# Optimization experiments

Measured on AMD Instinct MI355X. Metric: run time of the kernel, lower is better.

## Reference

```python
import jax, jax.numpy as jnp
import numpy as np

MASK_BIAS = 2.0
TEMPERATURE = 1.0


def setup_inputs() -> dict:
    key = jax.random.key(0)
    k1, k2, k3 = jax.random.split(key, 3)
    B, C, D, H, W = 2, 128, 48, 96, 96
    feat = jax.random.normal(k1, (B, C, D, H, W), dtype=jnp.float32)
    mask = jax.random.uniform(k2, (B, 1, D, H, W), dtype=jnp.float32)
    w_attn = jax.random.normal(k3, (C,), dtype=jnp.float32) * (1.0 / np.sqrt(C))
    return {"feat": feat, "mask": mask, "w_attn": w_attn}


def reference(feat, mask, w_attn):
    B, C = feat.shape[:2]
    # 1x1x1 conv with 1 output channel, no bias == channel dot product
    logits = jnp.einsum('bcdhw,c->bdhw', feat, w_attn)  # [B, D, H, W]
    logits = logits + MASK_BIAS * jnp.clip(mask[:, 0], 0.0, 1.0)
    w = jax.nn.softmax((logits / TEMPERATURE).reshape(B, -1), axis=-1)  # [B, N]
    feat_flat = feat.reshape(B, C, -1)  # [B, C, N]
    return jnp.einsum('bcn,bn->bc', feat_flat, w)
```

## Files before the change

### kernel.cpp

```cpp
#include <hip/hip_runtime.h>

constexpr int C   = 128;
constexpr int N   = 48 * 96 * 96;
constexpr int B   = 2;
constexpr int P   = 256;
constexpr int BPB = N / P;
constexpr int G   = 16;
constexpr int NW  = 8;

template <int CTRL, int RM>
__device__ __forceinline__ float dpp_add_step(float x) {
    int y = __builtin_amdgcn_update_dpp(0, __float_as_int(x), CTRL, RM, 0xF, true);
    return x + __int_as_float(y);
}
__device__ __forceinline__ float wave_sum64(float x) {
    x = dpp_add_step<0xB1, 0xF>(x);
    x = dpp_add_step<0x4E, 0xF>(x);
    x = dpp_add_step<0x141, 0xF>(x);
    x = dpp_add_step<0x140, 0xF>(x);
    x = dpp_add_step<0x142, 0xA>(x);
    x = dpp_add_step<0x143, 0xC>(x);
    return x;
}

__global__ __launch_bounds__(512, 4) void attn_pool_pass1(
    const float* __restrict__ feat, const float* __restrict__ mask,
    const float* __restrict__ w, float* __restrict__ Sout, float* __restrict__ ml)
{
    const int tid = threadIdx.x;
    const int wv  = tid >> 6;
    const int t   = tid & 63;
    const int blk = blockIdx.x;
    const int b   = blk / BPB;
    const int n0  = (blk % BPB) * P;
    const int cb  = wv * G;

    const float* fbase = feat + (size_t)b * C * N + n0 + 4 * t;

    __shared__ float4 plog[NW][64];
    __shared__ float  rmax[NW];
    __shared__ float  rsum1;
    __shared__ float  SRed[NW][G];

    float4 f[G];
    float4 pl = make_float4(0.f, 0.f, 0.f, 0.f);
#pragma unroll
    for (int c = 0; c < G; ++c) {
        f[c] = *reinterpret_cast<const float4*>(fbase + (size_t)(cb + c) * N);
        const float wc = w[cb + c];
        pl.x = fmaf(f[c].x, wc, pl.x);
        pl.y = fmaf(f[c].y, wc, pl.y);
        pl.z = fmaf(f[c].z, wc, pl.z);
        pl.w = fmaf(f[c].w, wc, pl.w);
    }
    if (wv == 0) {
        float4 mv = *reinterpret_cast<const float4*>(mask + (size_t)b * N + n0 + 4 * t);
        pl.x += 2.f * fminf(fmaxf(mv.x, 0.f), 1.f);
        pl.y += 2.f * fminf(fmaxf(mv.y, 0.f), 1.f);
        pl.z += 2.f * fminf(fmaxf(mv.z, 0.f), 1.f);
        pl.w += 2.f * fminf(fmaxf(mv.w, 0.f), 1.f);
    }
    plog[wv][t] = pl;
    __syncthreads();

    float4 lg = plog[0][t];
#pragma unroll
    for (int g = 1; g < NW; ++g) {
        float4 q = plog[g][t];
        lg.x += q.x; lg.y += q.y; lg.z += q.z; lg.w += q.w;
    }

    float m = fmaxf(fmaxf(lg.x, lg.y), fmaxf(lg.z, lg.w));
#pragma unroll
    for (int off = 32; off; off >>= 1) m = fmaxf(m, __shfl_xor(m, off, 64));
    if (t == 0) rmax[wv] = m;
    __syncthreads();
    m = fmaxf(fmaxf(fmaxf(rmax[0], rmax[1]), fmaxf(rmax[2], rmax[3])),
              fmaxf(fmaxf(rmax[4], rmax[5]), fmaxf(rmax[6], rmax[7])));

    const float p0 = __expf(lg.x - m), p1 = __expf(lg.y - m);
    const float p2 = __expf(lg.z - m), p3 = __expf(lg.w - m);

    if (wv == 0) {
        float l = ((p0 + p1) + (p2 + p3));
#pragma unroll
        for (int off = 32; off; off >>= 1) l += __shfl_xor(l, off, 64);
        if (t == 0) rsum1 = l;
    }

#pragma unroll
    for (int c = 0; c < G; ++c) {
        float s = f[c].x * p0;
        s = fmaf(f[c].y, p1, s);
        s = fmaf(f[c].z, p2, s);
        s = fmaf(f[c].w, p3, s);
        s = wave_sum64(s);
        if (t == 63) SRed[wv][c] = s;
    }
    __syncthreads();

    if (tid < C) {
        Sout[(size_t)blk * C + tid] = SRed[tid >> 4][tid & 15];
    } else if (tid == C) {
        ml[2 * blk]     = m;
        ml[2 * blk + 1] = rsum1;
    }
}

__global__ __launch_bounds__(1024) void attn_pool_pass2(
    const float* __restrict__ S, const float* __restrict__ ml,
    float* __restrict__ out)
{
    const int b    = blockIdx.x;
    const int tid  = threadIdx.x;
    const int lane = tid & 63;
    const int wv   = tid >> 6;
    const float* mlb = ml + (size_t)b * BPB * 2;
    const float* Sb  = S  + (size_t)b * BPB * C;

    __shared__ float sc[BPB];
    __shared__ float redA[16], redB[16];
    __shared__ float racc[8][C];

    float m = -3.4e38f;
    for (int i = tid; i < BPB; i += 1024) m = fmaxf(m, mlb[2 * i]);
#pragma unroll
    for (int off = 32; off; off >>= 1) m = fmaxf(m, __shfl_xor(m, off, 64));
    if (lane == 0) redA[wv] = m;
    __syncthreads();
    float M = redA[0];
#pragma unroll
    for (int k = 1; k < 16; ++k) M = fmaxf(M, redA[k]);

    float z = 0.f;
    for (int i = tid; i < BPB; i += 1024) {
        float e = __expf(mlb[2 * i] - M);
        sc[i] = e;
        z = fmaf(mlb[2 * i + 1], e, z);
    }
#pragma unroll
    for (int off = 32; off; off >>= 1) z += __shfl_xor(z, off, 64);
    if (lane == 0) redB[wv] = z;
    __syncthreads();
    float Z = redB[0];
#pragma unroll
    for (int k = 1; k < 16; ++k) Z += redB[k];

    const int c  = tid & (C - 1);
    const int ck = tid >> 7;
    const int i0 = ck * (BPB / 8), i1 = i0 + (BPB / 8);
    float acc = 0.f;
    for (int i = i0; i < i1; ++i)
        acc = fmaf(Sb[(size_t)i * C + c], sc[i], acc);
    racc[ck][c] = acc;
    __syncthreads();

    if (tid < C) {
        float tot = 0.f;
#pragma unroll
        for (int k = 0; k < 8; ++k) tot += racc[k][tid];
        out[b * C + tid] = tot / Z;
    }
}

extern "C" void kernel_launch(void* const* d_in, const int* in_sizes, int n_in,
                              void* d_out, int out_size, void* d_ws, size_t ws_size,
                              hipStream_t stream)
{
    const float* feat = (const float*)d_in[0];
    const float* mask = (const float*)d_in[1];
    const float* w    = (const float*)d_in[2];

    float* Sout = (float*)d_ws;
    float* ml   = Sout + (size_t)B * BPB * C;

    attn_pool_pass1<<<B * BPB, 512, 0, stream>>>(feat, mask, w, Sout, ml);
    attn_pool_pass2<<<B, 1024, 0, stream>>>(Sout, ml, (float*)d_out);
}
```

Measured before the change: 589.4 us.

## Split final cross-block reduction into many-block partial pass plus tiny combine pass

The second pass previously ran only two blocks, each reducing all 1728 per-block partial vectors, so most of the GPU sat idle. It now launches 128 blocks. Each computes the global max, rescales its slice of partial sums and writes a partial vector, and a third tiny kernel sums these and divides by the normaliser. This exposes parallelism for the 1.7 MB of partial sums. In exchange it adds a kernel launch, and every block redundantly re-reads the ml array to recompute the max.

New measurement: 590.9 us. No clear change (+0.3%).

```diff
diff --git a/kernel.cpp b/kernel.cpp
--- a/kernel.cpp
+++ b/kernel.cpp
@@ -7,6 +7,8 @@
 constexpr int BPB = N / P;
 constexpr int G   = 16;
 constexpr int NW  = 8;
+constexpr int KB  = 64;
+constexpr int RPB = BPB / KB;
 
 template <int CTRL, int RM>
 __device__ __forceinline__ float dpp_add_step(float x) {
@@ -107,60 +109,80 @@
     }
 }
 
-__global__ __launch_bounds__(1024) void attn_pool_pass2(
+__global__ __launch_bounds__(256) void attn_pool_pass2(
     const float* __restrict__ S, const float* __restrict__ ml,
+    float* __restrict__ part)
+{
+    const int b    = blockIdx.x / KB;
+    const int k    = blockIdx.x % KB;
+    const int tid  = threadIdx.x;
+    const int lane = tid & 63;
+    const int wv   = tid >> 6;
+    const float2* mlb = (const float2*)(ml + (size_t)b * BPB * 2);
+    const float*  Sb  = S + (size_t)b * BPB * C;
+
+    __shared__ float red[4];
+    __shared__ float half1[C];
+
+    float m = -3.4e38f;
+    for (int i = tid; i < BPB; i += 256) m = fmaxf(m, mlb[i].x);
+#pragma unroll
+    for (int off = 32; off; off >>= 1) m = fmaxf(m, __shfl_xor(m, off, 64));
+    if (lane == 0) red[wv] = m;
+    __syncthreads();
+    const float M = fmaxf(fmaxf(red[0], red[1]), fmaxf(red[2], red[3]));
+
+    const int c = tid & (C - 1);
+    const int h = tid >> 7;
+    const int i0 = k * RPB;
+    float acc = 0.f;
+    for (int i = i0 + h; i < i0 + RPB; i += 2)
+        acc = fmaf(Sb[(size_t)i * C + c], __expf(mlb[i].x - M), acc);
+    if (h) half1[c] = acc;
+    __syncthreads();
+    if (!h) part[((size_t)b * KB + k) * C + c] = acc + half1[c];
+}
+
+__global__ __launch_bounds__(256) void attn_pool_pass3(
+    const float* __restrict__ part, const float* __restrict__ ml,
     float* __restrict__ out)
 {
     const int b    = blockIdx.x;
     const int tid  = threadIdx.x;
     const int lane = tid & 63;
     const int wv   = tid >> 6;
-    const float* mlb = ml + (size_t)b * BPB * 2;
-    const float* Sb  = S  + (size_t)b * BPB * C;
-
-    __shared__ float sc[BPB];
-    __shared__ float redA[16], redB[16];
-    __shared__ float racc[8][C];
+    const float2* mlb = (const float2*)(ml + (size_t)b * BPB * 2);
+
+    __shared__ float redA[4], redB[4];
+    __shared__ float half1[C];
 
     float m = -3.4e38f;
-    for (int i = tid; i < BPB; i += 1024) m = fmaxf(m, mlb[2 * i]);
+    for (int i = tid; i < BPB; i += 256) m = fmaxf(m, mlb[i].x);
 #pragma unroll
     for (int off = 32; off; off >>= 1) m = fmaxf(m, __shfl_xor(m, off, 64));
     if (lane == 0) redA[wv] = m;
     __syncthreads();
-    float M = redA[0];
-#pragma unroll
-    for (int k = 1; k < 16; ++k) M = fmaxf(M, redA[k]);
+    const float M = fmaxf(fmaxf(redA[0], redA[1]), fmaxf(redA[2], redA[3]));
 
     float z = 0.f;
-    for (int i = tid; i < BPB; i += 1024) {
-        float e = __expf(mlb[2 * i] - M);
-        sc[i] = e;
-        z = fmaf(mlb[2 * i + 1], e, z);
+    for (int i = tid; i < BPB; i += 256) {
+        float2 v = mlb[i];
+        z = fmaf(v.y, __expf(v.x - M), z);
     }
 #pragma unroll
     for (int off = 32; off; off >>= 1) z += __shfl_xor(z, off, 64);
     if (lane == 0) redB[wv] = z;
     __syncthreads();
-    float Z = redB[0];
-#pragma unroll
-    for (int k = 1; k < 16; ++k) Z += redB[k];
-
-    const int c  = tid & (C - 1);
-    const int ck = tid >> 7;
-    const int i0 = ck * (BPB / 8), i1 = i0 + (BPB / 8);
-    float acc = 0.f;
-    for (int i = i0; i < i1; ++i)
-        acc = fmaf(Sb[(size_t)i * C + c], sc[i], acc);
-    racc[ck][c] = acc;
-    __syncthreads();
-
-    if (tid < C) {
-        float tot = 0.f;
-#pragma unroll
-        for (int k = 0; k < 8; ++k) tot += racc[k][tid];
-        out[b * C + tid] = tot / Z;
-    }
+    const float Z = redB[0] + redB[1] + redB[2] + redB[3];
+
+    const int c = tid & (C - 1);
+    const int h = tid >> 7;
+    float tot = 0.f;
+    for (int k = h; k < KB; k += 2)
+        tot += part[((size_t)b * KB + k) * C + c];
+    if (h) half1[c] = tot;
+    __syncthreads();
+    if (!h) out[b * C + c] = (tot + half1[c]) / Z;
 }
 
 extern "C" void kernel_launch(void* const* d_in, const int* in_sizes, int n_in,
@@ -173,7 +195,9 @@
 
     float* Sout = (float*)d_ws;
     float* ml   = Sout + (size_t)B * BPB * C;
+    float* part = ml + (size_t)B * BPB * 2;
 
     attn_pool_pass1<<<B * BPB, 512, 0, stream>>>(feat, mask, w, Sout, ml);
-    attn_pool_pass2<<<B, 1024, 0, stream>>>(Sout, ml, (float*)d_out);
-}
+    attn_pool_pass2<<<B * KB, 256, 0, stream>>>(Sout, ml, part);
+    attn_pool_pass3<<<B, 256, 0, stream>>>(part, ml, (float*)d_out);
+}
```
